# Kernel optimization log

Measured on AMD Instinct MI355X. Metric: run time of the kernel, lower is better.

The kernel has to match this reference:

```python
import jax, jax.numpy as jnp
import numpy as np

D = 256  # rst_input_dim


def _gru_cell(x, h, W_ih, W_hh, b_ih, b_hh):
    # x, h: (..., D); W_*: (3D, D); PyTorch GRU gate order: r, z, n
    gi = x @ W_ih.T + b_ih          # (..., 3D)
    gh = h @ W_hh.T + b_hh
    i_r, i_z, i_n = jnp.split(gi, 3, axis=-1)
    h_r, h_z, h_n = jnp.split(gh, 3, axis=-1)
    r = jax.nn.sigmoid(i_r + h_r)
    z = jax.nn.sigmoid(i_z + h_z)
    n = jnp.tanh(i_n + r * h_n)
    return (1.0 - z) * n + z * h


def setup_inputs() -> dict:
    key = jax.random.key(0)
    ks = jax.random.split(key, 5)
    B, L = 32, 4096
    s = 1.0 / np.sqrt(D)
    return {
        "leaf_embeds": jax.random.normal(ks[0], (B, L, D), dtype=jnp.float32),
        "W_ih": jax.random.normal(ks[1], (3 * D, D), dtype=jnp.float32) * s,
        "W_hh": jax.random.normal(ks[2], (3 * D, D), dtype=jnp.float32) * s,
        "b_ih": jax.random.normal(ks[3], (3 * D,), dtype=jnp.float32) * s,
        "b_hh": jax.random.normal(ks[4], (3 * D,), dtype=jnp.float32) * s,
    }


def reference(leaf_embeds, W_ih, W_hh, b_ih, b_hh):
    # Post-order traversal of a perfect binary tree, batched level-by-level
    # (classic tree-RNN same-depth batching). Leaves: embed = EDU embedding,
    # hidden = zeros. Internal node: h0 = mean(h_left, h_right); run GRU over
    # the 2-step sequence [left_embed, right_embed]; out = mean of the two
    # GRU outputs; returned hidden = final GRU hidden.
    embeds = leaf_embeds                      # (B, N, D)
    hs = jnp.zeros_like(leaf_embeds)          # (B, N, D)
    n = embeds.shape[1]
    while n > 1:
        xL, xR = embeds[:, 0::2], embeds[:, 1::2]   # (B, n/2, D)
        hL, hR = hs[:, 0::2], hs[:, 1::2]
        h0 = 0.5 * (hL + hR)                         # mean of child hiddens
        h1 = _gru_cell(xL, h0, W_ih, W_hh, b_ih, b_hh)
        h2 = _gru_cell(xR, h1, W_ih, W_hh, b_ih, b_hh)
        embeds = 0.5 * (h1 + h2)                     # mean over seq outputs
        hs = h2
        n //= 2
    return embeds[:, 0]                              # (B, D): root embedding
```

## Files before the change

### kernel.cpp

```cpp
#include <hip/hip_runtime.h>
#include <hip/hip_bf16.h>
#include <stdint.h>

typedef _Float16 f16x8 __attribute__((ext_vector_type(8)));
typedef float    f32x4 __attribute__((ext_vector_type(4)));

#define GLDS16(gptr, lptr) \
  __builtin_amdgcn_global_load_lds((const __attribute__((address_space(1))) void*)(gptr), \
                                   (__attribute__((address_space(3))) void*)(lptr), 16, 0, 0)

__device__ __forceinline__ int tile_off(int rb, int c, int sub) {
    return ((rb * 4 + c) * 8 + sub) * 512;
}

__global__ __launch_bounds__(256) void prepack_weights(
    const float* __restrict__ Wih, const float* __restrict__ Whh,
    const float* __restrict__ bih, const float* __restrict__ bhh,
    _Float16* __restrict__ WP, float* __restrict__ BC)
{
    if (blockIdx.x == 2048) {
        int i = threadIdx.x;
        BC[i]       = bih[i] + bhh[i];
        BC[256 + i] = bih[256 + i] + bhh[256 + i];
        BC[512 + i] = bih[512 + i];
        BC[768 + i] = bhh[512 + i];
        return;
    }
    int idx = blockIdx.x * 256 + threadIdx.x;
    int j   = idx & 7;
    int nl  = (idx >> 3) & 63;
    int sub = (idx >> 9) & 7;
    int g   = (idx >> 12) & 3;
    int d0b = (idx >> 14) & 3;
    int c   = idx >> 16;
    int k = c * 64 + sub * 8 + j;
    int d = d0b * 64 + nl;
    float v = 0.f;
    if (g == 0)      v = (k < 256) ? Wih[d * 256 + k]         : Whh[d * 256 + (k - 256)];
    else if (g == 1) v = (k < 256) ? Wih[(256 + d) * 256 + k] : Whh[(256 + d) * 256 + (k - 256)];
    else if (g == 2) v = (k < 256) ? Wih[(512 + d) * 256 + k] : 0.f;
    else             v = (k >= 256) ? Whh[(512 + d) * 256 + (k - 256)] : 0.f;
    WP[idx] = (_Float16)v;
}

__global__ __launch_bounds__(256) void convert_split(
    const float* __restrict__ leaf, _Float16* __restrict__ XE, _Float16* __restrict__ XO)
{
    int g = blockIdx.x * 256 + threadIdx.x;
    int u = g & 31;
    int row = g >> 5;
    const float* src = leaf + (size_t)row * 256 + u * 8;
    float4 a = *(const float4*)src;
    float4 b = *(const float4*)(src + 4);
    f16x8 p;
    p[0] = (_Float16)a.x; p[1] = (_Float16)a.y; p[2] = (_Float16)a.z; p[3] = (_Float16)a.w;
    p[4] = (_Float16)b.x; p[5] = (_Float16)b.y; p[6] = (_Float16)b.z; p[7] = (_Float16)b.w;
    int ro = row >> 1;
    _Float16* dst = (row & 1) ? XO : XE;
    *(f16x8*)(dst + tile_off(ro >> 6, u >> 3, u & 7) + (ro & 63) * 8) = p;
}

template<int MT, bool SWIZ>
__global__ __launch_bounds__(256, (MT == 8) ? 2 : 3) void gru_cell(
    const _Float16* __restrict__ Xsrc,
    const _Float16* __restrict__ Hsrc,
    const _Float16* __restrict__ WP,
    const float* __restrict__ BC,
    _Float16* __restrict__ Hout,
    _Float16* __restrict__ Ee, _Float16* __restrict__ Eo, _Float16* __restrict__ HP,
    int M)
{
    (void)M;
    constexpr int AROW = MT * 16 * 8;
    constexpr int ASZ  = 8 * AROW;
    constexpr int BROW = 512;
    constexpr int BSZ  = 3 * 8 * BROW;
    __shared__ __align__(16) _Float16 Alds[2 * ASZ];
    __shared__ __align__(16) _Float16 Blds[2 * BSZ];

    const int tid  = threadIdx.x;
    int bm, d0b;
    if (SWIZ) {
        int xcd = blockIdx.x & 7, slot = blockIdx.x >> 3;
        d0b = slot & 3;
        bm  = (slot >> 2) * 8 + xcd;
    } else {
        bm = blockIdx.x >> 2; d0b = blockIdx.x & 3;
    }
    const int wave = tid >> 6, lane = tid & 63;
    const int quad = lane >> 4, lo = lane & 15;

    const bool has_h = (Hsrc != nullptr);
    const int nch = has_h ? 8 : 4;

    f32x4 acc[MT][4];
#pragma unroll
    for (int a = 0; a < MT; ++a)
#pragma unroll
        for (int b = 0; b < 4; ++b) acc[a][b] = (f32x4){0.f, 0.f, 0.f, 0.f};
    float hinv[MT][4];

    auto issueB = [&](int c) {
        const size_t cb = (size_t)(c * 4 + d0b) * 4;
        _Float16* dstb = Blds + (c & 1) * BSZ;
#pragma unroll
        for (int i = 0; i < 6; ++i) {
            int bi = wave * 6 + i;
            int slot = bi >> 3, sub = bi & 7;
            int g = (slot == 2) ? ((c < 4) ? 2 : 3) : slot;
            GLDS16(WP + ((cb + g) * 8 + sub) * 512 + lane * 8,
                   dstb + (slot * 8 + sub) * BROW);
        }
    };

    auto issueA = [&](int c) {
        const _Float16* base = (c < 4) ? Xsrc : Hsrc;
        const int cc = c & 3;
        _Float16* Ab = Alds + (c & 1) * ASZ;
        constexpr int ND = MT / 2;
#pragma unroll
        for (int i = 0; i < ND; ++i) {
            int ai = wave * ND + i;
            int sub = (MT == 8) ? (ai >> 1) : ai;
            int mh  = (MT == 8) ? (ai & 1) : 0;
            GLDS16(base + tile_off(bm * (MT / 4) + mh, cc, sub) + lane * 8,
                   Ab + sub * AROW + mh * 512);
        }
    };

    issueB(0);
    issueA(0);

    for (int c = 0; c < nch; ++c) {
        __syncthreads();
        if (c + 1 < nch) {
            issueB(c + 1);
            issueA(c + 1);
        }

        const _Float16* Bb = Blds + (c & 1) * BSZ;
        const _Float16* Ab = Alds + (c & 1) * ASZ;
#pragma unroll
        for (int ks = 0; ks < 2; ++ks) {
            const int subb = ks * 4 + quad;
            const _Float16* brow = Bb + subb * BROW + (wave * 16 + lo) * 8;
            f16x8 b0 = *(const f16x8*)(brow);
            f16x8 b1 = *(const f16x8*)(brow + 8 * BROW);
            f16x8 b2 = *(const f16x8*)(brow + 16 * BROW);
            f16x8 af[MT];
#pragma unroll
            for (int mt = 0; mt < MT; ++mt)
                af[mt] = *(const f16x8*)(Ab + subb * AROW + (mt * 16 + lo) * 8);
#pragma unroll
            for (int mt = 0; mt < MT; ++mt)
                acc[mt][0] = __builtin_amdgcn_mfma_f32_16x16x32_f16(af[mt], b0, acc[mt][0], 0, 0, 0);
#pragma unroll
            for (int mt = 0; mt < MT; ++mt)
                acc[mt][1] = __builtin_amdgcn_mfma_f32_16x16x32_f16(af[mt], b1, acc[mt][1], 0, 0, 0);
            if (c < 4) {
#pragma unroll
                for (int mt = 0; mt < MT; ++mt)
                    acc[mt][2] = __builtin_amdgcn_mfma_f32_16x16x32_f16(af[mt], b2, acc[mt][2], 0, 0, 0);
            } else {
#pragma unroll
                for (int mt = 0; mt < MT; ++mt)
                    acc[mt][3] = __builtin_amdgcn_mfma_f32_16x16x32_f16(af[mt], b2, acc[mt][3], 0, 0, 0);
            }
        }

        if (has_h && c == 4 + d0b) {
            const _Float16* Ab2 = Alds + (c & 1) * ASZ;
            const int colw = wave * 16 + lo;
            const int sub = colw >> 3, j = colw & 7;
#pragma unroll
            for (int mt = 0; mt < MT; ++mt)
#pragma unroll
                for (int r = 0; r < 4; ++r)
                    hinv[mt][r] = (float)Ab2[sub * AROW + (mt * 16 + quad * 4 + r) * 8 + j];
        }
    }

    const int ld = wave * 16 + lo;
    const int d  = d0b * 64 + ld;
    const float brz0 = BC[d];
    const float brz1 = BC[256 + d];
    const float bni  = BC[512 + d];
    const float bnh  = BC[768 + d];
    constexpr int SROW = 72;
    constexpr int PR   = MT * 8;
    __syncthreads();
#pragma unroll
    for (int mt = 0; mt < MT; ++mt) {
        const int lr0 = mt * 16 + quad * 4;
        float hq[4];
#pragma unroll
        for (int r = 0; r < 4; ++r) {
            float hin = has_h ? hinv[mt][r] : 0.f;
            float rg = 1.f / (1.f + __expf(-(acc[mt][0][r] + brz0)));
            float zg = 1.f / (1.f + __expf(-(acc[mt][1][r] + brz1)));
            float ex = __expf(2.f * (acc[mt][2][r] + bni + rg * (acc[mt][3][r] + bnh)));
            float nv = 1.f - 2.f / (ex + 1.f);
            hq[r] = (1.f - zg) * nv + zg * hin;
            int lr = lr0 + r;
            if (Hout) {
                Alds[lr * SROW + ld] = (_Float16)hq[r];
            } else {
                Alds[(((lr & 1) * PR) + (lr >> 1)) * SROW + ld] =
                    (_Float16)(0.5f * (hin + hq[r]));
            }
        }
        if (!Hout) {
            Alds[(2 * PR + (lr0 >> 1)) * SROW + ld]     = (_Float16)(0.5f * (hq[0] + hq[1]));
            Alds[(2 * PR + (lr0 >> 1) + 1) * SROW + ld] = (_Float16)(0.5f * (hq[2] + hq[3]));
        }
    }
    __syncthreads();

    if (Hout) {
        constexpr int NU = MT * 128;
#pragma unroll
        for (int i = 0; i < NU / 256; ++i) {
            int uid = i * 256 + tid;
            int r = uid & 63, sub = (uid >> 6) & 7, mh = uid >> 9;
            f16x8 v = *(const f16x8*)&Alds[(mh * 64 + r) * SROW + sub * 8];
            *(f16x8*)(Hout + tile_off(bm * (MT / 4) + mh, d0b, sub) + r * 8) = v;
        }
    } else {
        constexpr int NU = 3 * PR * 8;
        const int rbE  = (MT == 8) ? bm : (bm >> 1);
        const int roff = (MT == 8) ? 0 : (bm & 1) * 32;
#pragma unroll
        for (int i = 0; i < NU / 256; ++i) {
            int uid = i * 256 + tid;
            int pr   = uid & (PR - 1);
            int rest = uid / PR;
            int sub = rest & 7, buf = rest >> 3;
            f16x8 v = *(const f16x8*)&Alds[(buf * PR + pr) * SROW + sub * 8];
            _Float16* dst = (buf == 0) ? Ee : (buf == 1) ? Eo : HP;
            *(f16x8*)(dst + tile_off(rbE, d0b, sub) + (roff + pr) * 8) = v;
        }
    }
}

__global__ __launch_bounds__(256) void final_out(
    const _Float16* __restrict__ XE, const _Float16* __restrict__ XO,
    float* __restrict__ out)
{
    int i = blockIdx.x * 256 + threadIdx.x;
    int j = i >> 8, col = i & 255;
    const _Float16* src = (j & 1) ? XO : XE;
    int r = j >> 1;
    out[i] = (float)src[tile_off(0, col >> 6, (col >> 3) & 7) + r * 8 + (col & 7)];
}

extern "C" void kernel_launch(void* const* d_in, const int* in_sizes, int n_in,
                              void* d_out, int out_size, void* d_ws, size_t ws_size,
                              hipStream_t stream) {
    const float* leaf = (const float*)d_in[0];
    const float* Wih  = (const float*)d_in[1];
    const float* Whh  = (const float*)d_in[2];
    const float* bih  = (const float*)d_in[3];
    const float* bhh  = (const float*)d_in[4];

    char* ws = (char*)d_ws;
    _Float16* WPp = (_Float16*)ws;
    _Float16* XAe = (_Float16*)(ws + (1ull  << 20));
    _Float16* XAo = (_Float16*)(ws + (33ull << 20));
    _Float16* XBe = (_Float16*)(ws + (65ull << 20));
    _Float16* XBo = (_Float16*)(ws + (81ull << 20));
    _Float16* H1  = (_Float16*)(ws + (97ull << 20));
    _Float16* HPb = (_Float16*)(ws + (129ull << 20));
    float*    BCp = (float*)(ws + (145ull << 20));

    prepack_weights<<<2049, 256, 0, stream>>>(Wih, Whh, bih, bhh, WPp, BCp);
    convert_split<<<16384, 256, 0, stream>>>(leaf, XAe, XAo);

    _Float16 *XeC = XAe, *XoC = XAo, *XeN = XBe, *XoN = XBo;
    const _Float16* hp = nullptr;
    int M = 65536;
    for (int lev = 0; lev < 12; ++lev) {
        if (M >= 8192) {
            int grid = (M / 128) * 4;
            gru_cell<8, true><<<grid, 256, 0, stream>>>(XeC, hp, WPp, BCp,
                                                        H1, nullptr, nullptr, nullptr, M);
            gru_cell<8, true><<<grid, 256, 0, stream>>>(XoC, H1, WPp, BCp,
                                                        nullptr, XeN, XoN, HPb, M);
        } else {
            int nbm = (M + 63) / 64;
            int grid = nbm * 4;
            if ((nbm & 7) == 0) {
                gru_cell<4, true><<<grid, 256, 0, stream>>>(XeC, hp, WPp, BCp,
                                                            H1, nullptr, nullptr, nullptr, M);
                gru_cell<4, true><<<grid, 256, 0, stream>>>(XoC, H1, WPp, BCp,
                                                            nullptr, XeN, XoN, HPb, M);
            } else {
                gru_cell<4, false><<<grid, 256, 0, stream>>>(XeC, hp, WPp, BCp,
                                                             H1, nullptr, nullptr, nullptr, M);
                gru_cell<4, false><<<grid, 256, 0, stream>>>(XoC, H1, WPp, BCp,
                                                             nullptr, XeN, XoN, HPb, M);
            }
        }
        hp = HPb;
        _Float16* t;
        t = XeC; XeC = XeN; XeN = t;
        t = XoC; XoC = XoN; XoN = t;
        M >>= 1;
    }
    final_out<<<32, 256, 0, stream>>>(XeC, XoC, (float*)d_out);
}
```

Before: 673.4 us.

## Deepen GRU GEMM pipeline to 4-stage half-chunk ring with explicit vmcnt waits

Splits each K chunk into two halves and stages them through a 4-slot LDS ring, issuing three halves ahead instead of one chunk. It replaces __syncthreads with explicit s_waitcnt vmcnt counts plus s_barrier, so loads for later stages stay in flight while MFMAs run on the current one. MFMA sections are wrapped in s_setprio to favour matrix issue. Both A and B LDS buffers keep the same total size. The hand-counted vmcnt values are fragile: if they do not match the per-thread loads issued per half, the kernel races, and the finer barrier cadence adds more synchronisation points.

```diff
diff --git a/kernel.cpp b/kernel.cpp
--- a/kernel.cpp
+++ b/kernel.cpp
@@ -8,6 +8,8 @@
 #define GLDS16(gptr, lptr) \
   __builtin_amdgcn_global_load_lds((const __attribute__((address_space(1))) void*)(gptr), \
                                    (__attribute__((address_space(3))) void*)(lptr), 16, 0, 0)
+
+#define WAITV(N) asm volatile("s_waitcnt vmcnt(" #N ")" ::: "memory")
 
 __device__ __forceinline__ int tile_off(int rb, int c, int sub) {
     return ((rb * 4 + c) * 8 + sub) * 512;
@@ -71,12 +73,12 @@
     int M)
 {
     (void)M;
-    constexpr int AROW = MT * 16 * 8;
-    constexpr int ASZ  = 8 * AROW;
-    constexpr int BROW = 512;
-    constexpr int BSZ  = 3 * 8 * BROW;
-    __shared__ __align__(16) _Float16 Alds[2 * ASZ];
-    __shared__ __align__(16) _Float16 Blds[2 * BSZ];
+    constexpr int AROW  = MT * 16 * 8;
+    constexpr int AHALF = 4 * AROW;
+    constexpr int BROW  = 512;
+    constexpr int BHALF = 12 * BROW;
+    __shared__ __align__(16) _Float16 Alds[4 * AHALF];
+    __shared__ __align__(16) _Float16 Blds[4 * BHALF];
 
     const int tid  = threadIdx.x;
     int bm, d0b;
@@ -91,7 +93,7 @@
     const int quad = lane >> 4, lo = lane & 15;
 
     const bool has_h = (Hsrc != nullptr);
-    const int nch = has_h ? 8 : 4;
+    const int NH = has_h ? 16 : 8;
 
     f32x4 acc[MT][4];
 #pragma unroll
@@ -100,83 +102,79 @@
         for (int b = 0; b < 4; ++b) acc[a][b] = (f32x4){0.f, 0.f, 0.f, 0.f};
     float hinv[MT][4];
 
-    auto issueB = [&](int c) {
+    auto issueHalf = [&](int h) {
+        const int hb = h & 3, par = h & 1, c = h >> 1;
         const size_t cb = (size_t)(c * 4 + d0b) * 4;
-        _Float16* dstb = Blds + (c & 1) * BSZ;
-#pragma unroll
-        for (int i = 0; i < 6; ++i) {
-            int bi = wave * 6 + i;
-            int slot = bi >> 3, sub = bi & 7;
+        _Float16* dstb = Blds + hb * BHALF;
+#pragma unroll
+        for (int i = 0; i < 3; ++i) {
+            int bi = wave * 3 + i;
+            int slot = bi >> 2, s = bi & 3;
             int g = (slot == 2) ? ((c < 4) ? 2 : 3) : slot;
-            GLDS16(WP + ((cb + g) * 8 + sub) * 512 + lane * 8,
-                   dstb + (slot * 8 + sub) * BROW);
-        }
-    };
-
-    auto issueA = [&](int c) {
+            GLDS16(WP + ((cb + g) * 8 + par * 4 + s) * 512 + lane * 8,
+                   dstb + (slot * 4 + s) * BROW);
+        }
         const _Float16* base = (c < 4) ? Xsrc : Hsrc;
         const int cc = c & 3;
-        _Float16* Ab = Alds + (c & 1) * ASZ;
-        constexpr int ND = MT / 2;
-#pragma unroll
-        for (int i = 0; i < ND; ++i) {
-            int ai = wave * ND + i;
-            int sub = (MT == 8) ? (ai >> 1) : ai;
-            int mh  = (MT == 8) ? (ai & 1) : 0;
-            GLDS16(base + tile_off(bm * (MT / 4) + mh, cc, sub) + lane * 8,
-                   Ab + sub * AROW + mh * 512);
+        _Float16* Ab = Alds + hb * AHALF;
+        constexpr int APW = MT / 4;
+#pragma unroll
+        for (int i = 0; i < APW; ++i) {
+            int ai = wave * APW + i;
+            int s  = (MT == 8) ? (ai >> 1) : ai;
+            int mh = (MT == 8) ? (ai & 1) : 0;
+            GLDS16(base + tile_off(bm * (MT / 4) + mh, cc, par * 4 + s) + lane * 8,
+                   Ab + s * AROW + mh * 512);
         }
     };
 
-    issueB(0);
-    issueA(0);
-
-    for (int c = 0; c < nch; ++c) {
-        __syncthreads();
-        if (c + 1 < nch) {
-            issueB(c + 1);
-            issueA(c + 1);
-        }
-
-        const _Float16* Bb = Blds + (c & 1) * BSZ;
-        const _Float16* Ab = Alds + (c & 1) * ASZ;
-#pragma unroll
-        for (int ks = 0; ks < 2; ++ks) {
-            const int subb = ks * 4 + quad;
-            const _Float16* brow = Bb + subb * BROW + (wave * 16 + lo) * 8;
-            f16x8 b0 = *(const f16x8*)(brow);
-            f16x8 b1 = *(const f16x8*)(brow + 8 * BROW);
-            f16x8 b2 = *(const f16x8*)(brow + 16 * BROW);
-            f16x8 af[MT];
+    issueHalf(0); issueHalf(1); issueHalf(2);
+
+    for (int h = 0; h < NH; ++h) {
+        if (h < NH - 2)       { if (MT == 8) WAITV(10); else WAITV(8); }
+        else if (h == NH - 2) { if (MT == 8) WAITV(5);  else WAITV(4); }
+        else                  WAITV(0);
+        __builtin_amdgcn_s_barrier();
+        __builtin_amdgcn_sched_barrier(0);
+        if (h + 3 < NH) issueHalf(h + 3);
+
+        const _Float16* Bb = Blds + (h & 3) * BHALF;
+        const _Float16* Ab = Alds + (h & 3) * AHALF;
+        const _Float16* brow = Bb + quad * BROW + (wave * 16 + lo) * 8;
+        f16x8 b0 = *(const f16x8*)(brow);
+        f16x8 b1 = *(const f16x8*)(brow + 4 * BROW);
+        f16x8 b2 = *(const f16x8*)(brow + 8 * BROW);
+        f16x8 af[MT];
+#pragma unroll
+        for (int mt = 0; mt < MT; ++mt)
+            af[mt] = *(const f16x8*)(Ab + quad * AROW + (mt * 16 + lo) * 8);
+        const int c = h >> 1;
+        __builtin_amdgcn_s_setprio(1);
+#pragma unroll
+        for (int mt = 0; mt < MT; ++mt)
+            acc[mt][0] = __builtin_amdgcn_mfma_f32_16x16x32_f16(af[mt], b0, acc[mt][0], 0, 0, 0);
+#pragma unroll
+        for (int mt = 0; mt < MT; ++mt)
+            acc[mt][1] = __builtin_amdgcn_mfma_f32_16x16x32_f16(af[mt], b1, acc[mt][1], 0, 0, 0);
+        if (c < 4) {
 #pragma unroll
             for (int mt = 0; mt < MT; ++mt)
-                af[mt] = *(const f16x8*)(Ab + subb * AROW + (mt * 16 + lo) * 8);
+                acc[mt][2] = __builtin_amdgcn_mfma_f32_16x16x32_f16(af[mt], b2, acc[mt][2], 0, 0, 0);
+        } else {
 #pragma unroll
             for (int mt = 0; mt < MT; ++mt)
-                acc[mt][0] = __builtin_amdgcn_mfma_f32_16x16x32_f16(af[mt], b0, acc[mt][0], 0, 0, 0);
+                acc[mt][3] = __builtin_amdgcn_mfma_f32_16x16x32_f16(af[mt], b2, acc[mt][3], 0, 0, 0);
+        }
+        __builtin_amdgcn_s_setprio(0);
+
+        if (has_h && c == 4 + d0b && (wave >> 1) == (h & 1)) {
+            const int colw = wave * 16 + lo;
+            const int sl = (colw >> 3) & 3, j = colw & 7;
 #pragma unroll
             for (int mt = 0; mt < MT; ++mt)
-                acc[mt][1] = __builtin_amdgcn_mfma_f32_16x16x32_f16(af[mt], b1, acc[mt][1], 0, 0, 0);
-            if (c < 4) {
-#pragma unroll
-                for (int mt = 0; mt < MT; ++mt)
-                    acc[mt][2] = __builtin_amdgcn_mfma_f32_16x16x32_f16(af[mt], b2, acc[mt][2], 0, 0, 0);
-            } else {
-#pragma unroll
-                for (int mt = 0; mt < MT; ++mt)
-                    acc[mt][3] = __builtin_amdgcn_mfma_f32_16x16x32_f16(af[mt], b2, acc[mt][3], 0, 0, 0);
-            }
-        }
-
-        if (has_h && c == 4 + d0b) {
-            const _Float16* Ab2 = Alds + (c & 1) * ASZ;
-            const int colw = wave * 16 + lo;
-            const int sub = colw >> 3, j = colw & 7;
-#pragma unroll
-            for (int mt = 0; mt < MT; ++mt)
 #pragma unroll
                 for (int r = 0; r < 4; ++r)
-                    hinv[mt][r] = (float)Ab2[sub * AROW + (mt * 16 + quad * 4 + r) * 8 + j];
+                    hinv[mt][r] = (float)Ab[sl * AROW + (mt * 16 + quad * 4 + r) * 8 + j];
         }
     }
 
```

Result: slower. 749.9 us (+11.4%).
